# Kernel tuning notes

Hardware: AMD Instinct MI355X
Metric: run time of the kernel (lower is better)

## Reference

```python
import jax, jax.numpy as jnp
import numpy as np

B, T, F, U, OUT_STEPS = 512, 48, 2048, 2048, 24


def setup_inputs() -> dict:
    key = jax.random.key(0)
    ks = jax.random.split(key, 4)
    s = 0.02  # small init scale keeps gates in a sane range
    return {
        "inputs": jax.random.normal(ks[0], (B, T, F), jnp.float32),
        "kernel": jax.random.normal(ks[1], (F, 4 * U), jnp.float32) * s,
        "rec_kernel": jax.random.normal(ks[2], (U, 4 * U), jnp.float32) * s,
        "bias": jnp.zeros((4 * U,), jnp.float32),
        "dense_w": jax.random.normal(ks[3], (U, F), jnp.float32) * s,
        "dense_b": jnp.zeros((F,), jnp.float32),
    }


def _lstm_step(h, c, x, kernel, rec_kernel, bias):
    # Keras LSTMCell: gate order i, f, c(g), o; sigmoid recurrent act, tanh act
    z = x @ kernel + h @ rec_kernel + bias  # [B, 4U]
    i, f, g, o = jnp.split(z, 4, axis=-1)
    c = jax.nn.sigmoid(f) * c + jax.nn.sigmoid(i) * jnp.tanh(g)
    h = jax.nn.sigmoid(o) * jnp.tanh(c)
    return h, c


def reference(inputs, kernel, rec_kernel, bias, dense_w, dense_b):
    Bsz = inputs.shape[0]
    Uh = rec_kernel.shape[0]
    h0 = jnp.zeros((Bsz, Uh), inputs.dtype)

    # warmup: run LSTM over the input window, keep final state
    def warm(carry, x_t):
        h, c = carry
        h, c = _lstm_step(h, c, x_t, kernel, rec_kernel, bias)
        return (h, c), None

    (h, c), _ = jax.lax.scan(warm, (h0, h0), jnp.swapaxes(inputs, 0, 1))
    pred0 = h @ dense_w + dense_b  # [B, F]

    def dec(carry, _):
        h, c, pred = carry
        h, c = _lstm_step(h, c, pred, kernel, rec_kernel, bias)
        pred = h @ dense_w + dense_b
        return (h, c, pred), pred

    _, preds = jax.lax.scan(dec, (h, c, pred0), None, length=OUT_STEPS - 1)
    preds = jnp.concatenate([pred0[None], preds], axis=0)  # [OUT, B, F]
    return jnp.transpose(preds, (1, 0, 2))  # [B, OUT, F]
```

## Files before the change

kernel.cpp:

```cpp
#include <hip/hip_runtime.h>
#include <hip/hip_bf16.h>
#include <cstddef>
#include <cstdint>

typedef __attribute__((ext_vector_type(8))) short short8;
typedef __attribute__((ext_vector_type(4))) float f32x4;
typedef unsigned short u16;
typedef unsigned int u32;

#define B_ 512
#define T_ 48
#define F_ 2048
#define U_ 2048
#define G4 8192
#define OT 24

__device__ __forceinline__ u16 f2bf(float f) {
    __hip_bfloat16 b = __float2bfloat16(f);
    return *reinterpret_cast<u16*>(&b);
}
__device__ __forceinline__ float bf2f(u16 v) {
    union { u32 u; float f; } c;
    c.u = ((u32)v) << 16;
    return c.f;
}

__device__ __forceinline__ void gl_lds16(const void* g, void* l) {
    __builtin_amdgcn_global_load_lds(
        (const __attribute__((address_space(1))) void*)g,
        (__attribute__((address_space(3))) void*)l, 16, 0, 0);
}

__device__ __forceinline__ void map_tile(int BM, int BN, int& m0, int& n0) {
    const int gx = gridDim.x, gy = gridDim.y;
    int lin = blockIdx.y * gx + blockIdx.x;
    const int nwg = gx * gy;
    const int sn = gx >> 3;
    const int EN = (sn >= 4) ? 4 : sn;
    const int EM = 4;
    bool ok = ((gx & 7) == 0) && ((gy & 3) == 0) && (sn < 4 || (sn & 3) == 0);
    if (ok) {
        int xcd = lin & 7, idx = lin >> 3;
        int epw = EM * EN;
        int e = idx / epw, r = idx % epw;
        int meb = gy / EM;
        int ne = e / meb, me = e % meb;
        int mi = r % EM, nli = r / EM;
        m0 = (me * EM + mi) * BM;
        n0 = (xcd * sn + ne * EN + nli) * BN;
    } else {
        if ((nwg & 7) == 0) {
            int q = nwg >> 3;
            lin = (lin & 7) * q + (lin >> 3);
        }
        m0 = (lin / gx) * BM;
        n0 = (lin % gx) * BN;
    }
}

template <int ILV>
__global__ void transpose_f32_bf16(const float* __restrict__ in,
                                   u16* __restrict__ out, int R, int C) {
    __shared__ float tile[32][33];
    int bx = blockIdx.x * 32;
    int by = blockIdx.y * 32;
    int tx = threadIdx.x, ty = threadIdx.y;
#pragma unroll
    for (int j = 0; j < 32; j += 8)
        tile[ty + j][tx] = in[(size_t)(by + ty + j) * C + bx + tx];
    __syncthreads();
#pragma unroll
    for (int j = 0; j < 32; j += 8) {
        int cidx = bx + ty + j;
        int orow = ILV ? (((cidx & 2047) << 2) | (cidx >> 11)) : cidx;
        out[(size_t)orow * R + by + tx] = f2bf(tile[tx][ty + j]);
    }
}

__global__ void cvt_bf16(const float* __restrict__ in, u16* __restrict__ out, long n) {
    long i = ((long)blockIdx.x * blockDim.x + threadIdx.x) * 4;
    if (i >= n) return;
    f32x4 v = *(const f32x4*)(in + i);
    ushort4 o;
    o.x = f2bf(v[0]); o.y = f2bf(v[1]); o.z = f2bf(v[2]); o.w = f2bf(v[3]);
    *(ushort4*)(out + i) = o;
}

__global__ void cvt_x_tmajor(const float* __restrict__ x, u16* __restrict__ xbf) {
    long i = ((long)blockIdx.x * blockDim.x + threadIdx.x) * 4;
    int f = (int)(i & (F_ - 1));
    long bt = i >> 11;
    int t = (int)(bt % T_);
    int b = (int)(bt / T_);
    f32x4 v = *(const f32x4*)(x + i);
    ushort4 o;
    o.x = f2bf(v[0]); o.y = f2bf(v[1]); o.z = f2bf(v[2]); o.w = f2bf(v[3]);
    *(ushort4*)(xbf + ((size_t)t * B_ + b) * F_ + f) = o;
}

__global__ void make_bias4(const float* __restrict__ bias, float* __restrict__ b4) {
    int n = blockIdx.x * 256 + threadIdx.x;
    int g = n & 3, u = n >> 2;
    b4[n] = bias[g * 2048 + u];
}

__global__ void bcomb_k(const u16* __restrict__ W4kT, const float* __restrict__ bd,
                        const float* __restrict__ bias4, float* __restrict__ bc) {
    int lane = threadIdx.x & 63, wid = threadIdx.x >> 6;
    int n = blockIdx.x * 4 + wid;
    const u16* row = W4kT + (size_t)n * U_;
    float s = 0.f;
    for (int j0 = lane * 8; j0 < U_; j0 += 512) {
        short8 v = *(const short8*)&row[j0];
#pragma unroll
        for (int e = 0; e < 8; ++e) s += bd[j0 + e] * bf2f((u16)v[e]);
    }
#pragma unroll
    for (int o = 32; o; o >>= 1) s += __shfl_down(s, o);
    if (lane == 0) bc[n] = bias4[n] + s;
}

template <int BM, int BN, int WR, int WC, int TPB, int NBUF>
__device__ __forceinline__ void gpipe(const u16* __restrict__ A, long lda,
                                      const u16* __restrict__ B, int K,
                                      int m0, int n0, int tid, u16* lds,
                                      f32x4 (&acc)[BM / WR / 16][BN / WC / 16]) {
    constexpr int BK = 64;
    constexpr int MF = BM / WR / 16, NF = BN / WC / 16;
    constexpr int TILE = (BM + BN) * BK;
    constexpr int LA = BM * BK / (TPB * 8);
    constexpr int LB = BN * BK / (TPB * 8);
    constexpr int LPS = LA + LB;
    static_assert((NBUF == 3 && (LPS == 4 || LPS == 6)) ||
                  (NBUF == 2 && (LPS == 6 || LPS == 8)), "vmcnt table");
    const int lane = tid & 63, wid = tid >> 6;
    const int wr = wid / WC, wc = wid % WC;
    const int r16 = lane & 15, kg = lane >> 4;
    const int kpar = wid & 1;
    const int NT = K / BK;

    auto stage = [&](int t) {
        if (t >= NT) return;
        const u16* Abase = A + (size_t)m0 * lda + (size_t)t * BK;
        const u16* Bbase = B + (size_t)n0 * (size_t)K + (size_t)t * BK;
        u16* dst = lds + (t % NBUF) * TILE;
#pragma unroll
        for (int i = 0; i < LA; ++i) {
            int idx = i * TPB + tid;
            int r = idx >> 3, sl = idx & 7;
            gl_lds16(Abase + (size_t)r * lda + ((sl ^ (r & 7)) * 8), dst + idx * 8);
        }
        u16* dstB = dst + BM * BK;
#pragma unroll
        for (int i = 0; i < LB; ++i) {
            int idx = i * TPB + tid;
            int r = idx >> 3, sl = idx & 7;
            gl_lds16(Bbase + (size_t)r * (size_t)K + ((sl ^ (r & 7)) * 8), dstB + idx * 8);
        }
    };
    auto compute = [&](int t) {
        const u16* Ab = lds + (t % NBUF) * TILE;
        const u16* Bb = Ab + BM * BK;
        __builtin_amdgcn_s_setprio(1);
#pragma unroll
        for (int ks2 = 0; ks2 < 2; ++ks2) {
            const int ks = ks2 ^ kpar;
            short8 af[MF], bf[NF];
#pragma unroll
            for (int mi = 0; mi < MF; ++mi) {
                int row = wr * (BM / WR) + mi * 16 + r16;
                int s = (ks * 4 + kg) ^ (row & 7);
                af[mi] = *(const short8*)&Ab[row * BK + s * 8];
            }
#pragma unroll
            for (int ni = 0; ni < NF; ++ni) {
                int row = wc * (BN / WC) + ni * 16 + r16;
                int s = (ks * 4 + kg) ^ (row & 7);
                bf[ni] = *(const short8*)&Bb[row * BK + s * 8];
            }
#pragma unroll
            for (int mi = 0; mi < MF; ++mi)
#pragma unroll
                for (int ni = 0; ni < NF; ++ni)
                    acc[mi][ni] = __builtin_amdgcn_mfma_f32_16x16x32_bf16(
                        af[mi], bf[ni], acc[mi][ni], 0, 0, 0);
        }
        __builtin_amdgcn_s_setprio(0);
    };

    if constexpr (NBUF == 3) {
        stage(0);
        stage(1);
        for (int t = 0; t < NT; ++t) {
            stage(t + 2);
            if (t + 2 < NT) {
                if constexpr (LPS == 6)
                    asm volatile("s_waitcnt vmcnt(12)\ns_barrier" ::: "memory");
                else
                    asm volatile("s_waitcnt vmcnt(8)\ns_barrier" ::: "memory");
            } else if (t + 1 < NT) {
                if constexpr (LPS == 6)
                    asm volatile("s_waitcnt vmcnt(6)\ns_barrier" ::: "memory");
                else
                    asm volatile("s_waitcnt vmcnt(4)\ns_barrier" ::: "memory");
            } else {
                asm volatile("s_waitcnt vmcnt(0)\ns_barrier" ::: "memory");
            }
            compute(t);
            asm volatile("s_barrier" ::: "memory");
        }
    } else {
        stage(0);
        for (int t = 0; t < NT; ++t) {
            stage(t + 1);
            if (t + 1 < NT) {
                if constexpr (LPS == 8)
                    asm volatile("s_waitcnt vmcnt(8)\ns_barrier" ::: "memory");
                else
                    asm volatile("s_waitcnt vmcnt(6)\ns_barrier" ::: "memory");
            } else {
                asm volatile("s_waitcnt vmcnt(0)\ns_barrier" ::: "memory");
            }
            compute(t);
            asm volatile("s_barrier" ::: "memory");
        }
    }
}

template <int BM, int BN, int WR, int WC, int TPB, int NBUF, int CM, int BIAS, int OUTM>
__global__ __launch_bounds__(TPB) void gemm3(
    const u16* __restrict__ A1, long lda1, const u16* __restrict__ B1, int K1,
    const void* __restrict__ Ci, long ldci, const float* __restrict__ bias,
    void* __restrict__ Co, long ldc, void* __restrict__ Co2, long ldc2) {
    __shared__ __align__(16) u16 lds[NBUF * (BM + BN) * 64];
    int m0, n0;
    map_tile(BM, BN, m0, n0);
    const int tid = threadIdx.x;

    f32x4 acc[BM / WR / 16][BN / WC / 16] = {};
    gpipe<BM, BN, WR, WC, TPB, NBUF>(A1, lda1, B1, K1, m0, n0, tid, lds, acc);

    const int lane = tid & 63, wid = tid >> 6;
    const int wr = wid / WC, wc = wid % WC, r16 = lane & 15, rg = lane >> 4;
#pragma unroll
    for (int ni = 0; ni < BN / WC / 16; ++ni) {
        int col = n0 + wc * (BN / WC) + ni * 16 + r16;
        float bv = BIAS ? bias[col] : 0.f;
#pragma unroll
        for (int mi = 0; mi < BM / WR / 16; ++mi) {
#pragma unroll
            for (int r = 0; r < 4; ++r) {
                int row = m0 + wr * (BM / WR) + mi * 16 + rg * 4 + r;
                float v = acc[mi][ni][r] + bv;
                if constexpr (CM == 2) v += bf2f(((const u16*)Ci)[(size_t)row * ldci + col]);
                if constexpr (OUTM == 0) ((float*)Co)[(size_t)row * ldc + col] = v;
                if constexpr (OUTM == 1) ((u16*)Co)[(size_t)row * ldc + col] = f2bf(v);
                if constexpr (OUTM == 2) {
                    int t = row >> 9, b = row & 511;
                    ((float*)Co)[((size_t)b * OT + t) * F_ + col] = v;
                }
                if constexpr (OUTM == 3) {
                    ((float*)Co)[(size_t)row * ldc + col] = v;
                    ((u16*)Co2)[(size_t)row * ldc2 + col] = f2bf(v);
                }
            }
        }
    }
}

template <int MODE>
__global__ __launch_bounds__(512) void step128(
    const u16* __restrict__ hin, const u16* __restrict__ Wstep,
    const u16* __restrict__ zx_cur, const float* __restrict__ addv,
    float* __restrict__ c, u16* __restrict__ hout,
    const u16* __restrict__ A2, const u16* __restrict__ B2) {
    __shared__ __align__(16) u16 lds[3 * 256 * 64];
    float* zt = (float*)lds;
    const int tid = threadIdx.x;
    const int bid = blockIdx.x;
    const int xcd = bid & 7, idx = bid >> 3;
    const int n0 = (xcd * 8 + (idx & 7)) * 128;
    const int m0 = (idx >> 3) * 128;

    f32x4 acc[4][2] = {};
    gpipe<128, 128, 2, 4, 512, 3>(hin, U_, Wstep, U_, m0, n0, tid, lds, acc);
    if constexpr (MODE == 2)
        gpipe<128, 128, 2, 4, 512, 3>(A2, F_, B2, F_, m0, n0, tid, lds, acc);

    {
        const int lane = tid & 63, wid = tid >> 6;
        const int wr = wid >> 2, wc = wid & 3, r16 = lane & 15, rg = lane >> 4;
#pragma unroll
        for (int mi = 0; mi < 4; ++mi)
#pragma unroll
            for (int ni = 0; ni < 2; ++ni)
#pragma unroll
                for (int r = 0; r < 4; ++r)
                    zt[(wr * 64 + mi * 16 + rg * 4 + r) * 132 + wc * 32 + ni * 16 + r16] =
                        acc[mi][ni][r];
    }
    __syncthreads();

    const int row = tid >> 5, ul = tid & 31;
    const int ug = (n0 >> 2) + ul;
#pragma unroll
    for (int j = 0; j < 8; ++j) {
        int rr = j * 16 + row;
        f32x4 zv = *(const f32x4*)&zt[rr * 132 + 4 * ul];
        float zi = zv[0], zf = zv[1], zg = zv[2], zo = zv[3];
        if constexpr (MODE == 0) {
            ushort4 zb = *(const ushort4*)&zx_cur[(size_t)(m0 + rr) * G4 + n0 + 4 * ul];
            zi += bf2f(zb.x); zf += bf2f(zb.y); zg += bf2f(zb.z); zo += bf2f(zb.w);
        } else {
            f32x4 bv = *(const f32x4*)&addv[n0 + 4 * ul];
            zi += bv[0]; zf += bv[1]; zg += bv[2]; zo += bv[3];
        }
        size_t ci = (size_t)(m0 + rr) * U_ + ug;
        float si = 1.f / (1.f + __expf(-zi));
        float sf = 1.f / (1.f + __expf(-zf));
        float so = 1.f / (1.f + __expf(-zo));
        float cc = sf * c[ci] + si * tanhf(zg);
        c[ci] = cc;
        hout[ci] = f2bf(so * tanhf(cc));
    }
}

extern "C" void kernel_launch(void* const* d_in, const int* in_sizes, int n_in,
                              void* d_out, int out_size, void* d_ws, size_t ws_size,
                              hipStream_t stream) {
    const float* x = (const float*)d_in[0];
    const float* Wk = (const float*)d_in[1];
    const float* Wr = (const float*)d_in[2];
    const float* bias = (const float*)d_in[3];
    const float* Wd = (const float*)d_in[4];
    const float* bd = (const float*)d_in[5];
    float* out = (float*)d_out;

    u16* xbf = (u16*)d_out;

    auto pad = [](size_t s) { return (s + 255) & ~(size_t)255; };
    const size_t szW4 = (size_t)G4 * U_ * 2;
    const size_t szDT = (size_t)U_ * F_ * 2;
    const size_t szB4 = (size_t)G4 * 4;
    const size_t szH = (size_t)OT * B_ * U_ * 2;
    const size_t szHP = (size_t)B_ * U_ * 2;
    const size_t szC = (size_t)B_ * U_ * 4;
    const size_t szZX1 = (size_t)B_ * G4 * 2;
    const size_t SLOT = (size_t)B_ * U_;

    const size_t needMain = pad(szW4) * 3 + pad(szDT) * 2 + pad(szB4) * 2 +
                            pad(szH) + pad(szHP) * 2 + pad(szC) + pad(szZX1);
    const int path = ws_size >= needMain ? 1 : 0;

    char* p = (char*)d_ws;
    auto alloc = [&](size_t bytes) { void* r = p; p += (bytes + 255) & ~(size_t)255; return r; };

    dim3 tb32(32, 8);

    if (path == 1) {
        u16* W4kT = (u16*)alloc(szW4);
        u16* W4rT = (u16*)alloc(szW4);
        u16* W4cT = (u16*)alloc(szW4);
        u16* dT = (u16*)alloc(szDT);
        u16* dbf = (u16*)alloc(szDT);
        float* bias4 = (float*)alloc(szB4);
        float* bc4 = (float*)alloc(szB4);
        u16* H = (u16*)alloc(szH);
        u16* hp0 = (u16*)alloc(szHP);
        u16* hp1 = (u16*)alloc(szHP);
        float* c = (float*)alloc(szC);

        size_t avail = ws_size - (size_t)(p - (char*)d_ws);
        int chunk = (int)(avail / szZX1);
        if (chunk > T_) chunk = T_;
        u16* ZX = (u16*)alloc((size_t)chunk * szZX1);

        cvt_x_tmajor<<<(B_ * T_ * F_ / 4 + 255) / 256, 256, 0, stream>>>(x, xbf);
        transpose_f32_bf16<1><<<dim3(G4 / 32, F_ / 32), tb32, 0, stream>>>(Wk, W4kT, F_, G4);
        transpose_f32_bf16<1><<<dim3(G4 / 32, U_ / 32), tb32, 0, stream>>>(Wr, W4rT, U_, G4);
        transpose_f32_bf16<0><<<dim3(F_ / 32, U_ / 32), tb32, 0, stream>>>(Wd, dT, U_, F_);
        cvt_bf16<<<(U_ * F_ / 4 + 255) / 256, 256, 0, stream>>>(Wd, dbf, (long)U_ * F_);
        make_bias4<<<G4 / 256, 256, 0, stream>>>(bias, bias4);
        bcomb_k<<<G4 / 4, 256, 0, stream>>>(W4kT, bd, bias4, bc4);

        gemm3<256, 256, 2, 4, 512, 2, 2, 0, 1><<<dim3(U_ / 256, G4 / 256), 512, 0, stream>>>(
            W4kT, U_, dbf, F_, W4rT, U_, nullptr, W4cT, U_, nullptr, 0);

        hipMemsetAsync(c, 0, szC, stream);
        hipMemsetAsync(hp0, 0, szHP, stream);

        for (int t0 = 0; t0 < T_; t0 += chunk) {
            int nc = chunk < T_ - t0 ? chunk : T_ - t0;
            gemm3<256, 256, 2, 4, 512, 2, 0, 1, 1>
                <<<dim3(G4 / 256, nc * B_ / 256), 512, 0, stream>>>(
                    xbf + (size_t)t0 * B_ * F_, F_, W4kT, F_, nullptr, 0,
                    bias4, ZX, G4, nullptr, 0);
            for (int t = t0; t < t0 + nc; ++t) {
                const u16* hin = (t & 1) ? hp1 : hp0;
                u16* hout = (t == T_ - 1) ? H : ((t & 1) ? hp0 : hp1);
                step128<0><<<256, 512, 0, stream>>>(
                    hin, W4rT, ZX + (size_t)(t - t0) * B_ * G4, nullptr,
                    c, hout, nullptr, nullptr);
            }
        }
        for (int t = 1; t < OT; ++t) {
            step128<1><<<256, 512, 0, stream>>>(
                H + (size_t)(t - 1) * SLOT, W4cT, nullptr, bc4,
                c, H + (size_t)t * SLOT, nullptr, nullptr);
        }
        gemm3<256, 256, 2, 4, 512, 2, 0, 1, 2><<<dim3(F_ / 256, OT * B_ / 256), 512, 0, stream>>>(
            H, U_, dT, U_, nullptr, 0, bd, out, F_, nullptr, 0);
    } else {
        u16* W4kT = (u16*)alloc(szW4);
        u16* W4rT = (u16*)alloc(szW4);
        u16* dT = (u16*)alloc(szDT);
        float* bias4 = (float*)alloc(szB4);
        u16* hp0 = (u16*)alloc(szHP);
        u16* hp1 = (u16*)alloc(szHP);
        u16* pred = (u16*)alloc(szHP);
        float* c = (float*)alloc(szC);

        cvt_x_tmajor<<<(B_ * T_ * F_ / 4 + 255) / 256, 256, 0, stream>>>(x, xbf);
        transpose_f32_bf16<1><<<dim3(G4 / 32, F_ / 32), tb32, 0, stream>>>(Wk, W4kT, F_, G4);
        transpose_f32_bf16<1><<<dim3(G4 / 32, U_ / 32), tb32, 0, stream>>>(Wr, W4rT, U_, G4);
        transpose_f32_bf16<0><<<dim3(F_ / 32, U_ / 32), tb32, 0, stream>>>(Wd, dT, U_, F_);
        make_bias4<<<G4 / 256, 256, 0, stream>>>(bias, bias4);
        hipMemsetAsync(c, 0, szC, stream);
        hipMemsetAsync(hp0, 0, szHP, stream);

        u16* hin = hp0;
        u16* hout = hp1;
        for (int t = 0; t < T_; ++t) {
            step128<2><<<256, 512, 0, stream>>>(
                hin, W4rT, nullptr, bias4, c, hout,
                xbf + (size_t)t * B_ * F_, W4kT);
            u16* tmp = hin; hin = hout; hout = tmp;
        }
        gemm3<64, 128, 2, 2, 256, 3, 0, 1, 3><<<dim3(F_ / 128, B_ / 64), 256, 0, stream>>>(
            hin, U_, dT, U_, nullptr, 0, bd, out, (long)OT * F_, pred, U_);
        for (int t = 1; t < OT; ++t) {
            step128<2><<<256, 512, 0, stream>>>(
                hin, W4rT, nullptr, bias4, c, hout, pred, W4kT);
            u16* tmp = hin; hin = hout; hout = tmp;
            gemm3<64, 128, 2, 2, 256, 3, 0, 1, 3><<<dim3(F_ / 128, B_ / 64), 256, 0, stream>>>(
                hin, U_, dT, U_, nullptr, 0, bd, out + (size_t)t * F_, (long)OT * F_, pred, U_);
        }
    }
}
```

Baseline: 3.071 ms.

## Add quarter-staged double-buffered 8-wave GEMM for input projection

Adds a new 256x256 tile bf16 MFMA GEMM kernel that splits each K-tile into four quadrants and interleaves the next tile's global-to-LDS loads with compute, using fine-grained vmcnt waits, barriers and setprio. It replaces the generic gemm3 for the chunked input-projection GEMM (x @ Wk + bias). The goal is to hide global memory latency better in the largest GEMM. The cost is more complex synchronization, with a risk of barrier overhead or subtle ordering bugs.

```diff
diff --git a/kernel.cpp b/kernel.cpp
--- a/kernel.cpp
+++ b/kernel.cpp
@@ -268,6 +268,120 @@
     }
 }
 
+template <int BIAS, int OUTM>
+__global__ __launch_bounds__(512) void gemm8p(
+    const u16* __restrict__ A, long lda, const u16* __restrict__ Bm, int K,
+    const float* __restrict__ bias, void* __restrict__ Co, long ldc) {
+    constexpr int BK = 64;
+    __shared__ __align__(16) u16 lds[2 * 512 * BK];
+    int m0, n0;
+    map_tile(256, 256, m0, n0);
+    const int tid = threadIdx.x;
+    const int lane = tid & 63, wid = tid >> 6;
+    const int wm = wid >> 2, wn = wid & 3;
+    const int r16 = lane & 15, kg = lane >> 4;
+    const int NT = K / BK;
+
+    auto stageA = [&](int T, int half) {
+        u16* buf = lds + (T & 1) * 512 * BK;
+#pragma unroll
+        for (int i = 0; i < 2; ++i) {
+            int l = i * 512 + tid;
+            int s = l >> 3, sl = l & 7;
+            int pr = (s & 63) + ((s >> 6) << 7) + half * 64;
+            gl_lds16(A + (size_t)(m0 + pr) * lda + T * BK + ((sl ^ (pr & 7)) * 8),
+                     buf + pr * BK + sl * 8);
+        }
+    };
+    auto stageB = [&](int T, int half) {
+        u16* buf = lds + (T & 1) * 512 * BK + 256 * BK;
+#pragma unroll
+        for (int i = 0; i < 2; ++i) {
+            int l = i * 512 + tid;
+            int s = l >> 3, sl = l & 7;
+            int pr = (s & 31) + ((s >> 5) << 6) + half * 32;
+            gl_lds16(Bm + (size_t)(n0 + pr) * (size_t)K + T * BK + ((sl ^ (pr & 7)) * 8),
+                     buf + pr * BK + sl * 8);
+        }
+    };
+
+    f32x4 acc[8][4] = {};
+
+    stageA(0, 0); stageB(0, 0); stageB(0, 1); stageA(0, 1);
+    asm volatile("s_waitcnt vmcnt(0)\ns_barrier" ::: "memory");
+
+    for (int t = 0; t < NT; ++t) {
+        const u16* Ab = lds + (t & 1) * 512 * BK;
+        const u16* Bb = Ab + 256 * BK;
+        const bool more = (t + 1 < NT);
+#pragma unroll
+        for (int q = 0; q < 4; ++q) {
+            const int qr = q >> 1, qc = q & 1;
+            if (more) {
+                if (q == 0) stageA(t + 1, 0);
+                else if (q == 1) stageB(t + 1, 0);
+                else if (q == 2) stageB(t + 1, 1);
+                else stageA(t + 1, 1);
+            }
+            asm volatile("s_barrier" ::: "memory");
+            __builtin_amdgcn_s_setprio(1);
+#pragma unroll
+            for (int ks = 0; ks < 2; ++ks) {
+                short8 af[4], bf[2];
+#pragma unroll
+                for (int fi = 0; fi < 4; ++fi) {
+                    int row = wm * 128 + qr * 64 + fi * 16 + r16;
+                    int s = (ks * 4 + kg) ^ (row & 7);
+                    af[fi] = *(const short8*)&Ab[row * BK + s * 8];
+                }
+#pragma unroll
+                for (int fj = 0; fj < 2; ++fj) {
+                    int row = wn * 64 + qc * 32 + fj * 16 + r16;
+                    int s = (ks * 4 + kg) ^ (row & 7);
+                    bf[fj] = *(const short8*)&Bb[row * BK + s * 8];
+                }
+#pragma unroll
+                for (int fi = 0; fi < 4; ++fi)
+#pragma unroll
+                    for (int fj = 0; fj < 2; ++fj)
+                        acc[qr * 4 + fi][qc * 2 + fj] =
+                            __builtin_amdgcn_mfma_f32_16x16x32_bf16(
+                                af[fi], bf[fj], acc[qr * 4 + fi][qc * 2 + fj], 0, 0, 0);
+            }
+            __builtin_amdgcn_s_setprio(0);
+            if (q == 0) {
+                if (more) asm volatile("s_waitcnt vmcnt(4)\ns_barrier" ::: "memory");
+                else      asm volatile("s_waitcnt vmcnt(2)\ns_barrier" ::: "memory");
+            } else if (q == 1) {
+                if (more) asm volatile("s_waitcnt vmcnt(4)\ns_barrier" ::: "memory");
+                else      asm volatile("s_waitcnt vmcnt(0)\ns_barrier" ::: "memory");
+            } else if (q == 2) {
+                asm volatile("s_barrier" ::: "memory");
+            } else {
+                if (more) asm volatile("s_waitcnt vmcnt(4)\ns_barrier" ::: "memory");
+                else      asm volatile("s_barrier" ::: "memory");
+            }
+        }
+    }
+
+    const int rg = lane >> 4;
+#pragma unroll
+    for (int ni = 0; ni < 4; ++ni) {
+        int col = n0 + wn * 64 + ni * 16 + r16;
+        float bv = BIAS ? bias[col] : 0.f;
+#pragma unroll
+        for (int mi = 0; mi < 8; ++mi) {
+#pragma unroll
+            for (int r = 0; r < 4; ++r) {
+                int row = m0 + wm * 128 + mi * 16 + rg * 4 + r;
+                float v = acc[mi][ni][r] + bv;
+                if constexpr (OUTM == 0) ((float*)Co)[(size_t)row * ldc + col] = v;
+                if constexpr (OUTM == 1) ((u16*)Co)[(size_t)row * ldc + col] = f2bf(v);
+            }
+        }
+    }
+}
+
 template <int MODE>
 __global__ __launch_bounds__(512) void step128(
     const u16* __restrict__ hin, const u16* __restrict__ Wstep,
@@ -391,10 +505,8 @@
 
         for (int t0 = 0; t0 < T_; t0 += chunk) {
             int nc = chunk < T_ - t0 ? chunk : T_ - t0;
-            gemm3<256, 256, 2, 4, 512, 2, 0, 1, 1>
-                <<<dim3(G4 / 256, nc * B_ / 256), 512, 0, stream>>>(
-                    xbf + (size_t)t0 * B_ * F_, F_, W4kT, F_, nullptr, 0,
-                    bias4, ZX, G4, nullptr, 0);
+            gemm8p<1, 1><<<dim3(G4 / 256, nc * B_ / 256), 512, 0, stream>>>(
+                xbf + (size_t)t0 * B_ * F_, F_, W4kT, F_, bias4, ZX, G4);
             for (int t = t0; t < t0 + nc; ++t) {
                 const u16* hin = (t & 1) ? hp1 : hp0;
                 u16* hout = (t == T_ - 1) ? H : ((t & 1) ? hp0 : hp1);
```

Result: no change. 3.042 ms (-1.0%).
